# Kernel tuning notes

Hardware: AMD Instinct MI355X
Metric: run time of the kernel (lower is better)

The kernel has to match this reference:

```python
import jax, jax.numpy as jnp
import numpy as np

SEQ_LEN = 1
INPUT = 2048
HIDDEN = 2048
CLASSES = 10
K = int(np.floor(np.sqrt(HIDDEN)))            # avgKernelSize = 45
NUM_EH = (HIDDEN - K) // K + 1                # 45 pooled features
LENGTHS = (32, 128, 512)                      # EHlengths (window sizes)
EST_DIM = NUM_EH * len(LENGTHS) * 2           # mean + variance per (feature, window)
B = 8192


def setup_inputs() -> dict:
    key = jax.random.key(0)
    ks = jax.random.split(key, 7)
    s = 1.0 / np.sqrt(HIDDEN)
    u = lambda k, shape: jax.random.uniform(k, shape, jnp.float32, -s, s)
    return {
        "x": jax.random.normal(ks[0], (B, SEQ_LEN, INPUT), jnp.float32),
        "W_ih": u(ks[1], (HIDDEN, INPUT)),
        "W_hh": u(ks[2], (HIDDEN, HIDDEN)),
        "b_ih": u(ks[3], (HIDDEN,)),
        "b_hh": u(ks[4], (HIDDEN,)),
        "W_lin": u(ks[5], (CLASSES, HIDDEN + EST_DIM)),
        "b_lin": u(ks[6], (CLASSES,)),
    }


def _sliding_stats(pooled):
    """Causal sliding-window mean/variance over the batch/stream axis.

    pooled: (B, F). Returns (B, F, J, 2) with [..., 0]=mean, [..., 1]=var.
    This is the exact quantity the VarEH exponential histograms approximate
    (streaming mean/variance over the last L elements added).
    """
    n = pooled.shape[0]
    cs = jnp.cumsum(pooled, axis=0)
    cs2 = jnp.cumsum(pooled * pooled, axis=0)
    idx = jnp.arange(n)
    outs = []
    for L in LENGTHS:  # small fixed set of window lengths
        zpad = jnp.zeros((L,) + pooled.shape[1:], pooled.dtype)
        cs_l = jnp.concatenate([zpad, cs], axis=0)[:n]
        cs2_l = jnp.concatenate([zpad, cs2], axis=0)[:n]
        cnt = jnp.minimum(idx + 1, L).astype(pooled.dtype)[:, None]
        m = (cs - cs_l) / cnt
        v = (cs2 - cs2_l) / cnt - m * m
        outs.append(jnp.stack([m, v], axis=-1))  # (B, F, 2)
    return jnp.stack(outs, axis=2)  # (B, F, J, 2)


def reference(x, W_ih, W_hh, b_ih, b_hh, W_lin, b_lin):
    b = x.shape[0]
    # Elman RNN, batch_first, h0 = 0. Precompute input projection for all steps.
    xw = jnp.einsum("bsi,hi->bsh", x, W_ih) + b_ih + b_hh  # (B, S, H)

    def step(h, xt):
        h = jnp.tanh(xt + h @ W_hh.T)
        return h, h

    h0 = jnp.zeros((b, HIDDEN), x.dtype)
    _, hs = jax.lax.scan(step, h0, jnp.swapaxes(xw, 0, 1))  # (S, B, H)
    rnn_out = hs[-1]  # (B, H); with seq_len=1 this equals squeeze(rnn_out)

    # AvgPool1d(kernel=K, stride=K) over hidden dim -> (B, NUM_EH)
    pooled = rnn_out[:, : NUM_EH * K].reshape(b, NUM_EH, K).mean(axis=-1)

    # Streaming mean/var estimates across the batch stream (VarEH semantics)
    est = _sliding_stats(pooled).reshape(b, EST_DIM)

    lin_in = jnp.concatenate([rnn_out, est], axis=1)  # (B, H + EST_DIM)
    logits = lin_in @ W_lin.T + b_lin
    return jax.nn.softmax(logits, axis=1)
```

## Files before the change

### kernel.cpp

```cpp
#include <hip/hip_runtime.h>
#include <hip/hip_bf16.h>
#include <math.h>

typedef short s16x8 __attribute__((ext_vector_type(8)));
typedef float f32x4 __attribute__((ext_vector_type(4)));

__device__ inline unsigned short f2bf(float x) {
    unsigned int u = __float_as_uint(x);
    unsigned int r = (u + 0x7fffu + ((u >> 16) & 1u)) >> 16;
    return (unsigned short)r;
}
__device__ inline float bf2f(unsigned short u) {
    return __uint_as_float(((unsigned int)u) << 16);
}

__device__ inline float fast_tanh(float x) {
    float e = __expf(2.0f * x);
    return 1.0f - 2.0f * __builtin_amdgcn_rcpf(e + 1.0f);
}

__global__ void cvtprep_kernel(const float* __restrict__ x,
                               const float* __restrict__ W_ih,
                               const float* __restrict__ W_lin,
                               unsigned short* __restrict__ xb,
                               unsigned short* __restrict__ wb,
                               unsigned short* __restrict__ wlb) {
    int blk = blockIdx.x;
    int tid = threadIdx.x;
    if (blk < 16384) {
        int i = blk * 256 + tid;
        float4 v = ((const float4*)x)[i];
        ushort4 o; o.x = f2bf(v.x); o.y = f2bf(v.y); o.z = f2bf(v.z); o.w = f2bf(v.w);
        ((ushort4*)xb)[i] = o;
    } else if (blk < 20480) {
        int i = (blk - 16384) * 256 + tid;
        float4 v = ((const float4*)W_ih)[i];
        ushort4 o; o.x = f2bf(v.x); o.y = f2bf(v.y); o.z = f2bf(v.z); o.w = f2bf(v.w);
        ((ushort4*)wb)[i] = o;
    } else {
        int idx = (blk - 20480) * 256 + tid;
        if (idx < 37376) {
            int c = idx / 2336, k = idx - c * 2336;
            float v = (c < 10 && k < 2318) ? W_lin[c * 2318 + k] : 0.f;
            wlb[idx] = f2bf(v);
        }
    }
}


#define MFMA_(a, b, c) __builtin_amdgcn_mfma_f32_16x16x32_bf16(a, b, c, 0, 0, 0)

__device__ inline s16x8 frag_ld(const unsigned short* hbase, int row, int ksub, int quad) {
    int slot = (ksub * 4 + quad) ^ (row & 7);
    return *(const s16x8*)(hbase + row * 64 + slot * 8);
}

__device__ inline void stage_u(const unsigned short* __restrict__ gmat, int half,
                               int rowoff, int kt, unsigned short* lmat, int tid) {
    int r = tid >> 3, s = tid & 7;
    int lr = rowoff + r;
    int ks = (s ^ (lr & 7)) << 3;
    const unsigned short* gp = gmat + (size_t)(half * 128 + lr) * 2048 + kt * 64 + ks;
    __builtin_amdgcn_global_load_lds(
        (const __attribute__((address_space(1))) void*)gp,
        (__attribute__((address_space(3))) void*)(lmat + half * 8192 + lr * 64 + s * 8),
        16, 0, 0);
}

#define LOAD_B(ks)                                                       \
    b0 = frag_ld(Bh, bco +  0 + mrow, (ks), quad);                       \
    b1 = frag_ld(Bh, bco + 16 + mrow, (ks), quad);                       \
    b2 = frag_ld(Bh, bco + 32 + mrow, (ks), quad);                       \
    b3 = frag_ld(Bh, bco + 48 + mrow, (ks), quad);

#define LOAD_A(h, ks)                                                    \
    af0 = frag_ld(Ah, (h) * 64 +  0 + mrow, (ks), quad);                 \
    af1 = frag_ld(Ah, (h) * 64 + 16 + mrow, (ks), quad);                 \
    af2 = frag_ld(Ah, (h) * 64 + 32 + mrow, (ks), quad);                 \
    af3 = frag_ld(Ah, (h) * 64 + 48 + mrow, (ks), quad);

#define MFMA_H(hh)                                                       \
    acc[(hh)*4 + 0][0] = MFMA_(af0, b0, acc[(hh)*4 + 0][0]);             \
    acc[(hh)*4 + 0][1] = MFMA_(af0, b1, acc[(hh)*4 + 0][1]);             \
    acc[(hh)*4 + 0][2] = MFMA_(af0, b2, acc[(hh)*4 + 0][2]);             \
    acc[(hh)*4 + 0][3] = MFMA_(af0, b3, acc[(hh)*4 + 0][3]);             \
    acc[(hh)*4 + 1][0] = MFMA_(af1, b0, acc[(hh)*4 + 1][0]);             \
    acc[(hh)*4 + 1][1] = MFMA_(af1, b1, acc[(hh)*4 + 1][1]);             \
    acc[(hh)*4 + 1][2] = MFMA_(af1, b2, acc[(hh)*4 + 1][2]);             \
    acc[(hh)*4 + 1][3] = MFMA_(af1, b3, acc[(hh)*4 + 1][3]);             \
    acc[(hh)*4 + 2][0] = MFMA_(af2, b0, acc[(hh)*4 + 2][0]);             \
    acc[(hh)*4 + 2][1] = MFMA_(af2, b1, acc[(hh)*4 + 2][1]);             \
    acc[(hh)*4 + 2][2] = MFMA_(af2, b2, acc[(hh)*4 + 2][2]);             \
    acc[(hh)*4 + 2][3] = MFMA_(af2, b3, acc[(hh)*4 + 2][3]);             \
    acc[(hh)*4 + 3][0] = MFMA_(af3, b0, acc[(hh)*4 + 3][0]);             \
    acc[(hh)*4 + 3][1] = MFMA_(af3, b1, acc[(hh)*4 + 3][1]);             \
    acc[(hh)*4 + 3][2] = MFMA_(af3, b2, acc[(hh)*4 + 3][2]);             \
    acc[(hh)*4 + 3][3] = MFMA_(af3, b3, acc[(hh)*4 + 3][3]);

#define PHASE_CORE(hh)                                                   \
    __builtin_amdgcn_s_barrier();                                        \
    asm volatile("s_waitcnt lgkmcnt(0)" ::: "memory");                   \
    __builtin_amdgcn_s_setprio(1);                                       \
    MFMA_H(hh);                                                          \
    __builtin_amdgcn_s_setprio(0);

__global__ __launch_bounds__(512) void gemm_tanh_kernel(
    const unsigned short* __restrict__ A, const unsigned short* __restrict__ Bm,
    const float* __restrict__ b_ih, const float* __restrict__ b_hh,
    unsigned short* __restrict__ Hb)
{
    __shared__ __align__(16) unsigned short lds[2][2][16384];

    const int tid  = threadIdx.x;
    const int lane = tid & 63;
    const int wave = tid >> 6;
    const int wgid = blockIdx.x;
    const int xcd  = wgid & 7;
    const int idx  = wgid >> 3;
    const int rblk = xcd * 4 + (idx & 3);
    const int cblk = idx >> 2;
    const int row0 = rblk * 256;
    const int col0 = cblk * 256;
    const int wm   = wave >> 2;
    const int wn   = wave & 3;
    const int quad = lane >> 4;
    const int mrow = lane & 15;
    const int NT   = 32;

    const unsigned short* Ag = A  + (size_t)row0 * 2048;
    const unsigned short* Bg = Bm + (size_t)col0 * 2048;

    f32x4 acc[8][4];
#pragma unroll
    for (int i = 0; i < 8; ++i)
#pragma unroll
        for (int j = 0; j < 4; ++j) acc[i][j] = f32x4{0.f, 0.f, 0.f, 0.f};

    stage_u(Ag, 0, 0,  0, lds[0][0], tid);  stage_u(Ag, 0, 64, 0, lds[0][0], tid);
    stage_u(Ag, 1, 0,  0, lds[0][0], tid);  stage_u(Ag, 1, 64, 0, lds[0][0], tid);
    stage_u(Bg, 0, 0,  0, lds[0][1], tid);  stage_u(Bg, 0, 64, 0, lds[0][1], tid);
    stage_u(Bg, 1, 0,  0, lds[0][1], tid);  stage_u(Bg, 1, 64, 0, lds[0][1], tid);
    stage_u(Bg, 0, 0,  1, lds[1][1], tid);  stage_u(Bg, 0, 64, 1, lds[1][1], tid);
    stage_u(Ag, 0, 0,  1, lds[1][0], tid);  stage_u(Ag, 1, 0,  1, lds[1][0], tid);
    asm volatile("s_waitcnt vmcnt(4)" ::: "memory");
    __builtin_amdgcn_s_barrier();

    for (int t = 0; t < NT; ++t) {
        const int buf = t & 1;
        unsigned short* LA  = lds[buf][0];
        unsigned short* LB  = lds[buf][1];
        unsigned short* NLA = lds[buf ^ 1][0];
        unsigned short* NLB = lds[buf ^ 1][1];
        const unsigned short* Ah = LA + wm * 8192;
        const unsigned short* Bh = LB + (wn >> 1) * 8192;
        const int bco = (wn & 1) * 64;

        s16x8 b0, b1, b2, b3;
        s16x8 af0, af1, af2, af3;

        LOAD_B(0);
        LOAD_A(0, 0);
        if (t + 1 < NT) {
            stage_u(Ag, 0, 64, t + 1, NLA, tid);
            stage_u(Ag, 1, 64, t + 1, NLA, tid);
            stage_u(Bg, 1, 0,  t + 1, NLB, tid);
            stage_u(Bg, 1, 64, t + 1, NLB, tid);
        }
        asm volatile("s_waitcnt lgkmcnt(4)" ::: "memory");
        PHASE_CORE(0);
        __builtin_amdgcn_s_barrier();

        LOAD_A(1, 0);
        PHASE_CORE(1);
        __builtin_amdgcn_s_barrier();

        LOAD_B(1);
        LOAD_A(0, 1);
        asm volatile("s_waitcnt lgkmcnt(4)" ::: "memory");
        PHASE_CORE(0);
        __builtin_amdgcn_s_barrier();

        LOAD_A(1, 1);
        if (t + 2 < NT) {
            stage_u(Bg, 0, 0,  t + 2, LB, tid);
            stage_u(Bg, 0, 64, t + 2, LB, tid);
            stage_u(Ag, 0, 0,  t + 2, LA, tid);
            stage_u(Ag, 1, 0,  t + 2, LA, tid);
        }
        PHASE_CORE(1);
        if (t + 2 < NT) {
            asm volatile("s_waitcnt vmcnt(4)" ::: "memory");
        } else if (t + 1 < NT) {
            asm volatile("s_waitcnt vmcnt(0)" ::: "memory");
        }
        __builtin_amdgcn_s_barrier();
    }

    float bias[4];
#pragma unroll
    for (int j = 0; j < 4; ++j) {
        int gc = col0 + wn * 64 + j * 16 + mrow;
        bias[j] = b_ih[gc] + b_hh[gc];
    }
#pragma unroll
    for (int i = 0; i < 8; ++i) {
#pragma unroll
        for (int rr = 0; rr < 4; ++rr) {
            int grow = row0 + wm * 128 + i * 16 + quad * 4 + rr;
#pragma unroll
            for (int j = 0; j < 4; ++j) {
                int gc = col0 + wn * 64 + j * 16 + mrow;
                float v = acc[i][j][rr] + bias[j];
                Hb[(size_t)grow * 2048 + gc] = f2bf(fast_tanh(v));
            }
        }
    }
}

__global__ __launch_bounds__(256) void pool_kernel(
    const unsigned short* __restrict__ Hb, float* __restrict__ pooled_t) {
    __shared__ unsigned short hs[8 * 2048];
    __shared__ float outs[45 * 8];
    int b0 = blockIdx.x * 8;
    int tid = threadIdx.x;
    const ushort4* src = (const ushort4*)(Hb + (size_t)b0 * 2048);
    ushort4* dst = (ushort4*)hs;
    for (int i = tid; i < 4096; i += 256) dst[i] = src[i];
    __syncthreads();
    for (int o = tid; o < 360; o += 256) {
        int f = o % 45, r = o / 45;
        const unsigned short* row = hs + r * 2048 + f * 45;
        float s = 0.f;
#pragma unroll
        for (int k = 0; k < 45; ++k) s += bf2f(row[k]);
        outs[f * 8 + r] = s * (1.0f / 45.0f);
    }
    __syncthreads();
    for (int o = tid; o < 360; o += 256) {
        int f = o >> 3, r = o & 7;
        pooled_t[f * 8192 + b0 + r] = outs[o];
    }
}

__global__ __launch_bounds__(256) void scan_kernel(
    const float* __restrict__ pooled_t,
    float* __restrict__ cs_t, float* __restrict__ cs2_t) {
    __shared__ float t1[256], t2[256];
    int f = blockIdx.x;
    int tid = threadIdx.x;
    const float* p = pooled_t + f * 8192;
    int base = tid * 32;
    float loc[32];
    float s1 = 0.f, s2 = 0.f;
#pragma unroll
    for (int i = 0; i < 32; ++i) {
        float v = p[base + i];
        loc[i] = v; s1 += v; s2 += v * v;
    }
    t1[tid] = s1; t2[tid] = s2;
    __syncthreads();
    for (int d = 1; d < 256; d <<= 1) {
        float a1 = (tid >= d) ? t1[tid - d] : 0.f;
        float a2 = (tid >= d) ? t2[tid - d] : 0.f;
        __syncthreads();
        t1[tid] += a1; t2[tid] += a2;
        __syncthreads();
    }
    float r1 = t1[tid] - s1, r2 = t2[tid] - s2;
    float* c1 = cs_t + f * 8192;
    float* c2 = cs2_t + f * 8192;
#pragma unroll
    for (int i = 0; i < 32; ++i) {
        float v = loc[i];
        r1 += v; r2 += v * v;
        c1[base + i] = r1; c2[base + i] = r2;
    }
}

#define ESTRIDE 290
__global__ __launch_bounds__(256) void final_kernel(
    const unsigned short* __restrict__ Hb,
    const float* __restrict__ cs_t, const float* __restrict__ cs2_t,
    const unsigned short* __restrict__ Wb, const float* __restrict__ b_lin,
    float* __restrict__ out) {
    __shared__ unsigned short Es[32 * ESTRIDE];
    __shared__ float comb[2 * 16 * 17];
    int tid = threadIdx.x;
    int lane = tid & 63;
    int wave = tid >> 6;
    int b0 = blockIdx.x * 32;

    for (int i = tid; i < 135 * 32; i += 256) {
        int fj = i >> 5, r = i & 31;
        int f = fj / 3, j = fj - 3 * f;
        int b = b0 + r;
        int L = (j == 0) ? 32 : (j == 1) ? 128 : 512;
        const float* c1 = cs_t + f * 8192;
        const float* c2 = cs2_t + f * 8192;
        float a1 = c1[b], a2 = c2[b];
        float p1 = 0.f, p2 = 0.f;
        if (b >= L) { p1 = c1[b - L]; p2 = c2[b - L]; }
        float cnt = (float)((b + 1 < L) ? (b + 1) : L);
        float m = (a1 - p1) / cnt;
        float v = (a2 - p2) / cnt - m * m;
        int d0 = f * 6 + j * 2;
        Es[r * ESTRIDE + d0]     = f2bf(m);
        Es[r * ESTRIDE + d0 + 1] = f2bf(v);
    }
    for (int i = tid; i < 32 * 18; i += 256) {
        int r = i / 18, d = 270 + i % 18;
        Es[r * ESTRIDE + d] = 0;
    }
    __syncthreads();

    const int t = wave >> 1;
    const int kh = wave & 1;
    const int quad = lane >> 4;
    const int mrow = lane & 15;
    const int rowt = b0 + t * 16;

    f32x4 acc = f32x4{0.f, 0.f, 0.f, 0.f};
    const unsigned short* arow = Hb + (size_t)(rowt + mrow) * 2048 + kh * 1024 + quad * 8;
    const unsigned short* brow = Wb + (size_t)mrow * 2336 + kh * 1024 + quad * 8;
#pragma unroll 4
    for (int k = 0; k < 1024; k += 32) {
        s16x8 a = *(const s16x8*)(arow + k);
        s16x8 b = *(const s16x8*)(brow + k);
        acc = __builtin_amdgcn_mfma_f32_16x16x32_bf16(a, b, acc, 0, 0, 0);
    }
    if (kh) {
        const unsigned short* erow = Es + (t * 16 + mrow) * ESTRIDE + quad * 8;
        const unsigned short* wrow = Wb + (size_t)mrow * 2336 + 2048 + quad * 8;
#pragma unroll
        for (int k = 0; k < 288; k += 32) {
            s16x8 a = *(const s16x8*)(erow + k);
            s16x8 b = *(const s16x8*)(wrow + k);
            acc = __builtin_amdgcn_mfma_f32_16x16x32_bf16(a, b, acc, 0, 0, 0);
        }
    }

    float* cb = comb + t * 272;
    if (kh == 0) {
#pragma unroll
        for (int r = 0; r < 4; ++r) cb[(quad * 4 + r) * 17 + mrow] = acc[r];
    }
    __syncthreads();
    if (kh == 1) {
#pragma unroll
        for (int r = 0; r < 4; ++r) cb[(quad * 4 + r) * 17 + mrow] += acc[r];
    }
    __syncthreads();

    if (tid < 32) {
        const float* base = comb + (tid >> 4) * 272 + (tid & 15) * 17;
        float lg[10];
        float mx = -1e30f;
#pragma unroll
        for (int c = 0; c < 10; ++c) {
            lg[c] = base[c] + b_lin[c];
            mx = fmaxf(mx, lg[c]);
        }
        float s = 0.f;
#pragma unroll
        for (int c = 0; c < 10; ++c) { lg[c] = expf(lg[c] - mx); s += lg[c]; }
        float inv = 1.0f / s;
#pragma unroll
        for (int c = 0; c < 10; ++c) out[(size_t)(b0 + tid) * 10 + c] = lg[c] * inv;
    }
}

extern "C" void kernel_launch(void* const* d_in, const int* in_sizes, int n_in,
                              void* d_out, int out_size, void* d_ws, size_t ws_size,
                              hipStream_t stream) {
    const float* x     = (const float*)d_in[0];
    const float* W_ih  = (const float*)d_in[1];
    const float* b_ih  = (const float*)d_in[3];
    const float* b_hh  = (const float*)d_in[4];
    const float* W_lin = (const float*)d_in[5];
    const float* b_lin = (const float*)d_in[6];
    float* out = (float*)d_out;

    char* ws = (char*)d_ws;
    unsigned short* xb  = (unsigned short*)(ws);
    unsigned short* wb  = (unsigned short*)(ws + 33554432);
    unsigned short* Hb  = (unsigned short*)(ws + 41943040);
    float* pooled_t     = (float*)(ws + 75497472);
    float* cs_t         = (float*)(ws + 76972032);
    float* cs2_t        = (float*)(ws + 78446592);
    unsigned short* wlb = (unsigned short*)(ws + 79921152);

    cvtprep_kernel<<<20626, 256, 0, stream>>>(x, W_ih, W_lin, xb, wb, wlb);
    gemm_tanh_kernel<<<256, 512, 0, stream>>>(xb, wb, b_ih, b_hh, Hb);
    pool_kernel<<<1024, 256, 0, stream>>>(Hb, pooled_t);
    scan_kernel<<<45, 256, 0, stream>>>(pooled_t, cs_t, cs2_t);
    final_kernel<<<256, 256, 0, stream>>>(Hb, cs_t, cs2_t, wlb, b_lin, out);
}
```

Baseline: 225.1 us.

## Split prefix scan into chunked blocks and shrink final kernel tile to 16 rows

```diff
diff --git a/kernel.cpp b/kernel.cpp
--- a/kernel.cpp
+++ b/kernel.cpp
@@ -244,19 +244,20 @@
 
 __global__ __launch_bounds__(256) void scan_kernel(
     const float* __restrict__ pooled_t,
-    float* __restrict__ cs_t, float* __restrict__ cs2_t) {
+    float* __restrict__ cs_t, float* __restrict__ cs2_t,
+    float* __restrict__ sums1, float* __restrict__ sums2) {
     __shared__ float t1[256], t2[256];
-    int f = blockIdx.x;
+    int f  = blockIdx.x >> 3;
+    int ch = blockIdx.x & 7;
     int tid = threadIdx.x;
-    const float* p = pooled_t + f * 8192;
-    int base = tid * 32;
-    float loc[32];
-    float s1 = 0.f, s2 = 0.f;
-#pragma unroll
-    for (int i = 0; i < 32; ++i) {
-        float v = p[base + i];
-        loc[i] = v; s1 += v; s2 += v * v;
-    }
+    const float* p = pooled_t + f * 8192 + ch * 1024;
+    float4 v = ((const float4*)p)[tid];
+    float q1[4], q2[4];
+    q1[0] = v.x;          q2[0] = v.x * v.x;
+    q1[1] = q1[0] + v.y;  q2[1] = q2[0] + v.y * v.y;
+    q1[2] = q1[1] + v.z;  q2[2] = q2[1] + v.z * v.z;
+    q1[3] = q1[2] + v.w;  q2[3] = q2[2] + v.w * v.w;
+    float s1 = q1[3], s2 = q2[3];
     t1[tid] = s1; t2[tid] = s2;
     __syncthreads();
     for (int d = 1; d < 256; d <<= 1) {
@@ -267,13 +268,14 @@
         __syncthreads();
     }
     float r1 = t1[tid] - s1, r2 = t2[tid] - s2;
-    float* c1 = cs_t + f * 8192;
-    float* c2 = cs2_t + f * 8192;
-#pragma unroll
-    for (int i = 0; i < 32; ++i) {
-        float v = loc[i];
-        r1 += v; r2 += v * v;
-        c1[base + i] = r1; c2[base + i] = r2;
+    float4 o1, o2;
+    o1.x = r1 + q1[0]; o1.y = r1 + q1[1]; o1.z = r1 + q1[2]; o1.w = r1 + q1[3];
+    o2.x = r2 + q2[0]; o2.y = r2 + q2[1]; o2.z = r2 + q2[2]; o2.w = r2 + q2[3];
+    ((float4*)(cs_t  + f * 8192 + ch * 1024))[tid] = o1;
+    ((float4*)(cs2_t + f * 8192 + ch * 1024))[tid] = o2;
+    if (tid == 255) {
+        sums1[f * 8 + ch] = t1[255];
+        sums2[f * 8 + ch] = t2[255];
     }
 }
 
@@ -281,25 +283,42 @@
 __global__ __launch_bounds__(256) void final_kernel(
     const unsigned short* __restrict__ Hb,
     const float* __restrict__ cs_t, const float* __restrict__ cs2_t,
+    const float* __restrict__ sums1, const float* __restrict__ sums2,
     const unsigned short* __restrict__ Wb, const float* __restrict__ b_lin,
     float* __restrict__ out) {
-    __shared__ unsigned short Es[32 * ESTRIDE];
-    __shared__ float comb[2 * 16 * 17];
+    __shared__ unsigned short Es[16 * ESTRIDE];
+    __shared__ float eb1[45 * 8], eb2[45 * 8];
+    __shared__ float comb[4][16][17];
     int tid = threadIdx.x;
     int lane = tid & 63;
     int wave = tid >> 6;
-    int b0 = blockIdx.x * 32;
-
-    for (int i = tid; i < 135 * 32; i += 256) {
-        int fj = i >> 5, r = i & 31;
+    int b0 = blockIdx.x * 16;
+
+    if (tid < 45) {
+        float a = 0.f, b = 0.f;
+#pragma unroll
+        for (int c = 0; c < 8; ++c) {
+            eb1[tid * 8 + c] = a; a += sums1[tid * 8 + c];
+            eb2[tid * 8 + c] = b; b += sums2[tid * 8 + c];
+        }
+    }
+    __syncthreads();
+
+    for (int i = tid; i < 135 * 16; i += 256) {
+        int fj = i >> 4, r = i & 15;
         int f = fj / 3, j = fj - 3 * f;
         int b = b0 + r;
         int L = (j == 0) ? 32 : (j == 1) ? 128 : 512;
         const float* c1 = cs_t + f * 8192;
         const float* c2 = cs2_t + f * 8192;
-        float a1 = c1[b], a2 = c2[b];
+        float a1 = c1[b] + eb1[f * 8 + (b >> 10)];
+        float a2 = c2[b] + eb2[f * 8 + (b >> 10)];
         float p1 = 0.f, p2 = 0.f;
-        if (b >= L) { p1 = c1[b - L]; p2 = c2[b - L]; }
+        if (b >= L) {
+            int ix = b - L;
+            p1 = c1[ix] + eb1[f * 8 + (ix >> 10)];
+            p2 = c2[ix] + eb2[f * 8 + (ix >> 10)];
+        }
         float cnt = (float)((b + 1 < L) ? (b + 1) : L);
         float m = (a1 - p1) / cnt;
         float v = (a2 - p2) / cnt - m * m;
@@ -307,29 +326,27 @@
         Es[r * ESTRIDE + d0]     = f2bf(m);
         Es[r * ESTRIDE + d0 + 1] = f2bf(v);
     }
-    for (int i = tid; i < 32 * 18; i += 256) {
+    for (int i = tid; i < 16 * 18; i += 256) {
         int r = i / 18, d = 270 + i % 18;
         Es[r * ESTRIDE + d] = 0;
     }
     __syncthreads();
 
-    const int t = wave >> 1;
-    const int kh = wave & 1;
+    const int kh = wave;
     const int quad = lane >> 4;
     const int mrow = lane & 15;
-    const int rowt = b0 + t * 16;
 
     f32x4 acc = f32x4{0.f, 0.f, 0.f, 0.f};
-    const unsigned short* arow = Hb + (size_t)(rowt + mrow) * 2048 + kh * 1024 + quad * 8;
-    const unsigned short* brow = Wb + (size_t)mrow * 2336 + kh * 1024 + quad * 8;
+    const unsigned short* arow = Hb + (size_t)(b0 + mrow) * 2048 + kh * 512 + quad * 8;
+    const unsigned short* brow = Wb + (size_t)mrow * 2336 + kh * 512 + quad * 8;
 #pragma unroll 4
-    for (int k = 0; k < 1024; k += 32) {
+    for (int k = 0; k < 512; k += 32) {
         s16x8 a = *(const s16x8*)(arow + k);
         s16x8 b = *(const s16x8*)(brow + k);
         acc = __builtin_amdgcn_mfma_f32_16x16x32_bf16(a, b, acc, 0, 0, 0);
     }
-    if (kh) {
-        const unsigned short* erow = Es + (t * 16 + mrow) * ESTRIDE + quad * 8;
+    if (kh == 3) {
+        const unsigned short* erow = Es + mrow * ESTRIDE + quad * 8;
         const unsigned short* wrow = Wb + (size_t)mrow * 2336 + 2048 + quad * 8;
 #pragma unroll
         for (int k = 0; k < 288; k += 32) {
@@ -339,25 +356,23 @@
         }
     }
 
-    float* cb = comb + t * 272;
-    if (kh == 0) {
-#pragma unroll
-        for (int r = 0; r < 4; ++r) cb[(quad * 4 + r) * 17 + mrow] = acc[r];
-    }
-    __syncthreads();
-    if (kh == 1) {
-#pragma unroll
-        for (int r = 0; r < 4; ++r) cb[(quad * 4 + r) * 17 + mrow] += acc[r];
-    }
-    __syncthreads();
-
-    if (tid < 32) {
-        const float* base = comb + (tid >> 4) * 272 + (tid & 15) * 17;
+#pragma unroll
+    for (int r = 0; r < 4; ++r) comb[kh][quad * 4 + r][mrow] = acc[r];
+    __syncthreads();
+
+    {
+        int r = tid >> 4, c = tid & 15;
+        float v = comb[0][r][c] + comb[1][r][c] + comb[2][r][c] + comb[3][r][c];
+        comb[0][r][c] = v;
+    }
+    __syncthreads();
+
+    if (tid < 16) {
         float lg[10];
         float mx = -1e30f;
 #pragma unroll
         for (int c = 0; c < 10; ++c) {
-            lg[c] = base[c] + b_lin[c];
+            lg[c] = comb[0][tid][c] + b_lin[c];
             mx = fmaxf(mx, lg[c]);
         }
         float s = 0.f;
@@ -388,10 +403,12 @@
     float* cs_t         = (float*)(ws + 76972032);
     float* cs2_t        = (float*)(ws + 78446592);
     unsigned short* wlb = (unsigned short*)(ws + 79921152);
+    float* sums1        = (float*)(ws + 79995904);
+    float* sums2        = (float*)(ws + 79997344);
 
     cvtprep_kernel<<<20626, 256, 0, stream>>>(x, W_ih, W_lin, xb, wb, wlb);
     gemm_tanh_kernel<<<256, 512, 0, stream>>>(xb, wb, b_ih, b_hh, Hb);
     pool_kernel<<<1024, 256, 0, stream>>>(Hb, pooled_t);
-    scan_kernel<<<45, 256, 0, stream>>>(pooled_t, cs_t, cs2_t);
-    final_kernel<<<256, 256, 0, stream>>>(Hb, cs_t, cs2_t, wlb, b_lin, out);
-}
+    scan_kernel<<<360, 256, 0, stream>>>(pooled_t, cs_t, cs2_t, sums1, sums2);
+    final_kernel<<<512, 256, 0, stream>>>(Hb, cs_t, cs2_t, sums1, sums2, wlb, b_lin, out);
+}
```

Result: faster. 217.8 us (-3.3%).
